# Optimization experiments

Hardware: AMD Instinct MI355X
Metric: run time of the kernel (lower is better)

## Reference

```python
import jax, jax.numpy as jnp
import numpy as np

N = 50000
E = 1_600_000
IN_C = 128
HID = 128
HEADS = 4
F_OUT = HID // HEADS  # 32
NEG_SLOPE = 0.2


def _glorot(key, shape):
    fan_in, fan_out = shape[0], shape[-1]
    lim = jnp.sqrt(6.0 / (fan_in + fan_out)).astype(jnp.float32)
    return jax.random.uniform(key, shape, jnp.float32, -lim, lim)


def setup_inputs() -> dict:
    key = jax.random.key(0)
    ks = jax.random.split(key, 12)
    x = jax.random.normal(ks[0], (N, IN_C), jnp.float32)
    edge_index = jax.random.randint(ks[1], (2, E), 0, N, jnp.int32)
    # layer 0 params
    W0 = _glorot(ks[2], (IN_C, HEADS * F_OUT))
    att_src0 = _glorot(ks[3], (HEADS, F_OUT))
    att_dst0 = _glorot(ks[4], (HEADS, F_OUT))
    b0 = jnp.zeros((HEADS * F_OUT,), jnp.float32)
    # layer 1 params
    W1 = _glorot(ks[5], (HID, HEADS * F_OUT))
    att_src1 = _glorot(ks[6], (HEADS, F_OUT))
    att_dst1 = _glorot(ks[7], (HEADS, F_OUT))
    b1 = jnp.zeros((HEADS * F_OUT,), jnp.float32)
    return {"x": x, "edge_index": edge_index,
            "W0": W0, "att_src0": att_src0, "att_dst0": att_dst0, "b0": b0,
            "W1": W1, "att_src1": att_src1, "att_dst1": att_dst1, "b1": b1}


def gat_conv(x, src, dst, W, att_src, att_dst, b):
    n = x.shape[0]
    h = (x @ W).reshape(n, HEADS, F_OUT)              # [N,H,F]
    a_s = jnp.einsum('nhf,hf->nh', h, att_src)        # [N,H]
    a_d = jnp.einsum('nhf,hf->nh', h, att_dst)        # [N,H]
    e = jax.nn.leaky_relu(a_s[src] + a_d[dst], NEG_SLOPE)   # [E,H]
    # segment softmax over destination-node neighborhoods
    e_max = jax.ops.segment_max(e, dst, num_segments=n)     # [N,H]
    e_exp = jnp.exp(e - e_max[dst])                          # [E,H]
    denom = jax.ops.segment_sum(e_exp, dst, num_segments=n)  # [N,H]
    denom = jnp.where(denom > 0, denom, 1.0)
    alpha = e_exp / denom[dst]                               # [E,H]
    msg = alpha[:, :, None] * h[src]                         # [E,H,F]
    out = jax.ops.segment_sum(msg, dst, num_segments=n)      # [N,H,F]
    return out.reshape(n, HEADS * F_OUT) + b


def reference(x, edge_index, W0, att_src0, att_dst0, b0, W1, att_src1, att_dst1, b1):
    src, dst = edge_index[0], edge_index[1]
    h = gat_conv(x, src, dst, W0, att_src0, att_dst0, b0)
    h = jax.nn.relu(h)  # dropout p=0.0 / eval mode -> identity
    out = gat_conv(h, src, dst, W1, att_src1, att_dst1, b1)
    return out
```

## Files before the change

kernel.cpp:

```cpp
#include <hip/hip_runtime.h>
#include <hip/hip_fp16.h>

#define N_NODES 50000
#define N_EDGES 1600000
#define NB 196
#define NBLK_H 256
#define CHUNK_H (N_EDGES / NBLK_H)
#define NBLK_S 512
#define CHUNK_S (N_EDGES / NBLK_S)
#define GEMM_BLOCKS 256

typedef _Float16 half8_t __attribute__((ext_vector_type(8)));
typedef _Float16 half2_t __attribute__((ext_vector_type(2)));
typedef float floatx4 __attribute__((ext_vector_type(4)));

#if defined(__has_builtin)
#  if __has_builtin(__builtin_amdgcn_fdot2)
#    define HAS_FDOT2 1
#  endif
#endif
#ifndef HAS_FDOT2
#  define HAS_FDOT2 0
#endif

__global__ __launch_bounds__(256) void edge_hist(const int* __restrict__ dst,
                                                 int* __restrict__ totals) {
    __shared__ int hist[NB];
    int t = threadIdx.x, b = blockIdx.x;
    if (t < NB) hist[t] = 0;
    __syncthreads();
    int s = b * CHUNK_H;
    for (int i = t; i < CHUNK_H; i += 256)
        atomicAdd(&hist[dst[s + i] >> 8], 1);
    __syncthreads();
    if (t < NB && hist[t]) atomicAdd(&totals[t], hist[t]);
}

__global__ __launch_bounds__(256) void gemm_mfma(const float* __restrict__ Xf,
                                                 const __half* __restrict__ Xh,
                                                 int in_half,
                                                 const float* __restrict__ W,
                                                 const float* __restrict__ att_s,
                                                 const float* __restrict__ att_d,
                                                 __half* __restrict__ H16,
                                                 float* __restrict__ as_out,
                                                 float* __restrict__ ad_out, int nrows,
                                                 const int* __restrict__ e_src,
                                                 const int* __restrict__ e_dst,
                                                 const int* __restrict__ btotal,
                                                 int* __restrict__ bcursor,
                                                 int* __restrict__ bucketed,
                                                 int with_scatter) {
    __shared__ __align__(16) char lds[49152];
    int t = threadIdx.x;
    if (with_scatter && blockIdx.x >= GEMM_BLOCKS) {
        int* recs   = reinterpret_cast<int*>(lds);
        int* srt    = reinterpret_cast<int*>(lds + 12800);
        int* bexcl  = reinterpret_cast<int*>(lds + 25600);
        int* hist   = reinterpret_cast<int*>(lds + 26624);
        int* lstart = reinterpret_cast<int*>(lds + 27648);
        int* curL   = reinterpret_cast<int*>(lds + 28672);
        int* gbase  = reinterpret_cast<int*>(lds + 29696);
        int b = blockIdx.x - GEMM_BLOCKS;
        int myTot = 0;
        if (t < NB) { myTot = btotal[t]; bexcl[t] = myTot; hist[t] = 0; }
        __syncthreads();
        for (int o = 1; o < NB; o <<= 1) {
            int v = (t < NB && t >= o) ? bexcl[t - o] : 0;
            __syncthreads();
            if (t < NB) bexcl[t] += v;
            __syncthreads();
        }
        if (t < NB) bexcl[t] -= myTot;
        int s0 = b * CHUNK_S;
        for (int i = t; i < CHUNK_S; i += 256) {
            unsigned sv = (unsigned)e_src[s0 + i], dv = (unsigned)e_dst[s0 + i];
            recs[i] = (int)((sv << 16) | dv);
            atomicAdd(&hist[dv >> 8], 1);
        }
        __syncthreads();
        int myCnt = (t < NB) ? hist[t] : 0;
        if (t < NB) lstart[t] = myCnt;
        __syncthreads();
        for (int o = 1; o < NB; o <<= 1) {
            int v = (t < NB && t >= o) ? lstart[t - o] : 0;
            __syncthreads();
            if (t < NB) lstart[t] += v;
            __syncthreads();
        }
        if (t < NB) {
            int ex = lstart[t] - myCnt;
            lstart[t] = ex;
            curL[t] = ex;
            gbase[t] = bexcl[t] + atomicAdd(&bcursor[t], myCnt);
        }
        __syncthreads();
        for (int i = t; i < CHUNK_S; i += 256) {
            int r = recs[i];
            int bk = (int)(((unsigned)r & 0xFFFFu) >> 8);
            int p = atomicAdd(&curL[bk], 1);
            srt[p] = r;
        }
        __syncthreads();
        for (int p = t; p < CHUNK_S; p += 256) {
            int r = srt[p];
            unsigned d = (unsigned)r & 0xFFFFu;
            int bk = (int)(d >> 8);
            int g = gbase[bk] + (p - lstart[bk]);
            bucketed[g] = (int)((((unsigned)r >> 16) << 8) | (d & 255u));
        }
        return;
    }
    char* Alds = lds;
    char* Wlds = lds + 16384;
    int lane = t & 63, wv_ = t >> 6;
    for (int p = 0; p < 16; ++p) {
        int flat = p * 256 + t;
        int k = flat >> 5;
        int n0 = (flat & 31) * 4;
        float4 wv = reinterpret_cast<const float4*>(W)[flat];
        const float* wf = reinterpret_cast<const float*>(&wv);
        #pragma unroll
        for (int i = 0; i < 4; ++i) {
            int n = n0 + i;
            int byte = (n * 256 + k * 2) ^ ((n & 7) << 4);
            *reinterpret_cast<__half*>(Wlds + byte) = __float2half(wf[i]);
        }
    }
    int col16 = lane & 15;
    float Asv[8], Adv[8];
    #pragma unroll
    for (int nt = 0; nt < 8; ++nt) {
        Asv[nt] = att_s[nt * 16 + col16];
        Adv[nt] = att_d[nt * 16 + col16];
    }
    int ksub = (lane >> 4) * 16;
    int rloc = wv_ * 16 + col16;
    int ntiles = (nrows + 63) / 64;
    for (int tile = blockIdx.x; tile < ntiles; tile += GEMM_BLOCKS) {
        int row0 = tile * 64;
        __syncthreads();
        for (int p = 0; p < 8; ++p) {
            int r = p * 8 + (t >> 5);
            int f4 = t & 31;
            int rr = row0 + r;
            uint2 hv = make_uint2(0, 0);
            if (rr < nrows) {
                if (in_half) {
                    hv = *reinterpret_cast<const uint2*>(Xh + (size_t)rr * 128 + f4 * 4);
                } else {
                    float4 xv = reinterpret_cast<const float4*>(Xf)[(size_t)rr * 32 + f4];
                    __half2* hp = reinterpret_cast<__half2*>(&hv);
                    hp[0] = __floats2half2_rn(xv.x, xv.y);
                    hp[1] = __floats2half2_rn(xv.z, xv.w);
                }
            }
            int byte = (r * 256 + f4 * 8) ^ ((r & 7) << 4);
            *reinterpret_cast<uint2*>(Alds + byte) = hv;
        }
        __syncthreads();
        half8_t afr[4];
        #pragma unroll
        for (int kb = 0; kb < 4; ++kb) {
            int byte = (rloc * 256 + kb * 64 + ksub) ^ ((rloc & 7) << 4);
            afr[kb] = *reinterpret_cast<half8_t*>(Alds + byte);
        }
        floatx4 acc[8];
        #pragma unroll
        for (int nt = 0; nt < 8; ++nt) {
            int n = nt * 16 + col16;
            floatx4 a = {0.f, 0.f, 0.f, 0.f};
            #pragma unroll
            for (int kb = 0; kb < 4; ++kb) {
                int byte = (n * 256 + kb * 64 + ksub) ^ ((n & 7) << 4);
                half8_t bfr = *reinterpret_cast<half8_t*>(Wlds + byte);
                a = __builtin_amdgcn_mfma_f32_16x16x32_f16(afr[kb], bfr, a, 0, 0, 0);
            }
            acc[nt] = a;
        }
        float ps[4][4], pd[4][4];
        #pragma unroll
        for (int reg = 0; reg < 4; ++reg)
            #pragma unroll
            for (int h = 0; h < 4; ++h) {
                ps[reg][h] = acc[2*h][reg] * Asv[2*h] + acc[2*h+1][reg] * Asv[2*h+1];
                pd[reg][h] = acc[2*h][reg] * Adv[2*h] + acc[2*h+1][reg] * Adv[2*h+1];
            }
        #pragma unroll
        for (int m = 1; m <= 8; m <<= 1)
            #pragma unroll
            for (int reg = 0; reg < 4; ++reg)
                #pragma unroll
                for (int h = 0; h < 4; ++h) {
                    ps[reg][h] += __shfl_xor(ps[reg][h], m);
                    pd[reg][h] += __shfl_xor(pd[reg][h], m);
                }
        int rbase = row0 + wv_ * 16 + (lane >> 4) * 4;
        #pragma unroll
        for (int reg = 0; reg < 4; ++reg) {
            int grow = rbase + reg;
            if (grow < nrows) {
                #pragma unroll
                for (int nt = 0; nt < 8; ++nt)
                    H16[(size_t)grow * 128 + nt * 16 + col16] = __float2half(acc[nt][reg]);
                if (col16 == 0) {
                    *reinterpret_cast<float4*>(as_out + (size_t)grow * 4) =
                        make_float4(ps[reg][0], ps[reg][1], ps[reg][2], ps[reg][3]);
                    *reinterpret_cast<float4*>(ad_out + (size_t)grow * 4) =
                        make_float4(pd[reg][0], pd[reg][1], pd[reg][2], pd[reg][3]);
                }
            }
        }
    }
}

__global__ __launch_bounds__(1024) void bucket_sort(const int* __restrict__ bucketed,
                                                    const int* __restrict__ btotal,
                                                    int* __restrict__ sorted_packed,
                                                    int* __restrict__ off) {
    __shared__ int bb[NB];
    __shared__ int cnt[256], scn[256], cur[256];
    int t = threadIdx.x, k = blockIdx.x;
    if (t < NB) bb[t] = btotal[t];
    if (t < 256) cnt[t] = 0;
    __syncthreads();
    for (int o = 1; o < NB; o <<= 1) {
        int v = (t < NB && t >= o) ? bb[t - o] : 0;
        __syncthreads();
        if (t < NB) bb[t] += v;
        __syncthreads();
    }
    int base = (k == 0) ? 0 : bb[k - 1];
    int end  = bb[k];
    int m = end - base;
    for (int i = t; i < m; i += 1024)
        atomicAdd(&cnt[bucketed[base + i] & 255], 1);
    __syncthreads();
    if (t < 256) scn[t] = cnt[t];
    __syncthreads();
    for (int o = 1; o < 256; o <<= 1) {
        int v = (t < 256 && t >= o) ? scn[t - o] : 0;
        __syncthreads();
        if (t < 256) scn[t] += v;
        __syncthreads();
    }
    if (t < 256) {
        int excl = scn[t] - cnt[t];
        cur[t] = base + excl;
        int node = k * 256 + t;
        if (node <= N_NODES) off[node] = base + excl;
    }
    __syncthreads();
    for (int i = t; i < m; i += 1024) {
        int rec = bucketed[base + i];
        int p = atomicAdd(&cur[rec & 255], 1);
        sorted_packed[p] = rec;
    }
}

__global__ __launch_bounds__(64, 8) void gat_aggregate_v4(const __half* __restrict__ H16,
                                                          const int* __restrict__ off,
                                                          const int* __restrict__ packed,
                                                          const float* __restrict__ asb,
                                                          const float* __restrict__ adb,
                                                          const float* __restrict__ bias,
                                                          float* __restrict__ OUTF,
                                                          __half* __restrict__ OUTH,
                                                          int n, int mode) {
    int wid = blockIdx.x;
    int lane = threadIdx.x;
    if (wid >= n) return;
    int s = off[wid], e = off[wid + 1];
    int q = lane >> 4;
    int sub = lane & 15;
    int head4 = (sub >> 2) * 4;
    int sub16 = sub * 16;
    float adv = adb[(size_t)wid * 4 + (sub >> 2)];
    const char* Hc = reinterpret_cast<const char*>(H16);
    const char* Ac = reinterpret_cast<const char*>(asb);
    float acc[8] = {0, 0, 0, 0, 0, 0, 0, 0};
    float den = 0.f;
    if (s < e) {
        int idx[4]; float sc[4];
        #pragma unroll
        for (int u = 0; u < 4; ++u) {
            int ii = s + q + u * 4;
            int jj = ii < e ? ii : s;
            idx[u] = packed[jj] & 0xFFFFFF00;
            sc[u] = *reinterpret_cast<const float*>(Ac + (idx[u] >> 4) + head4);
        }
        for (int i = s; i < e; i += 16) {
            uint4 h0 = *reinterpret_cast<const uint4*>(Hc + idx[0] + sub16);
            uint4 h1 = *reinterpret_cast<const uint4*>(Hc + idx[1] + sub16);
            uint4 h2 = *reinterpret_cast<const uint4*>(Hc + idx[2] + sub16);
            uint4 h3 = *reinterpret_cast<const uint4*>(Hc + idx[3] + sub16);
            float w[4];
            #pragma unroll
            for (int u = 0; u < 4; ++u) {
                float ev = sc[u] + adv; ev = fmaxf(ev, 0.2f * ev);
                w[u] = (i + q + u * 4 < e) ? __expf(ev) : 0.f;
            }
            #pragma unroll
            for (int u = 0; u < 4; ++u) {
                int ii = i + 16 + q + u * 4;
                int jj = ii < e ? ii : s;
                idx[u] = packed[jj] & 0xFFFFFF00;
                sc[u] = *reinterpret_cast<const float*>(Ac + (idx[u] >> 4) + head4);
            }
            den += (w[0] + w[1]) + (w[2] + w[3]);
#if HAS_FDOT2
            half2_t w01 = __builtin_bit_cast(half2_t, __builtin_amdgcn_cvt_pkrtz(w[0], w[1]));
            half2_t w23 = __builtin_bit_cast(half2_t, __builtin_amdgcn_cvt_pkrtz(w[2], w[3]));
            const uint* a0 = reinterpret_cast<const uint*>(&h0);
            const uint* a1 = reinterpret_cast<const uint*>(&h1);
            const uint* a2 = reinterpret_cast<const uint*>(&h2);
            const uint* a3 = reinterpret_cast<const uint*>(&h3);
            #pragma unroll
            for (int j = 0; j < 4; ++j) {
                uint p0 = __builtin_amdgcn_perm(a1[j], a0[j], 0x05040100u);
                uint p1 = __builtin_amdgcn_perm(a1[j], a0[j], 0x07060302u);
                uint r0 = __builtin_amdgcn_perm(a3[j], a2[j], 0x05040100u);
                uint r1 = __builtin_amdgcn_perm(a3[j], a2[j], 0x07060302u);
                acc[2*j]   = __builtin_amdgcn_fdot2(__builtin_bit_cast(half2_t, p0), w01,
                             __builtin_amdgcn_fdot2(__builtin_bit_cast(half2_t, r0), w23, acc[2*j],   false), false);
                acc[2*j+1] = __builtin_amdgcn_fdot2(__builtin_bit_cast(half2_t, p1), w01,
                             __builtin_amdgcn_fdot2(__builtin_bit_cast(half2_t, r1), w23, acc[2*j+1], false), false);
            }
#else
            const __half2* pa = reinterpret_cast<const __half2*>(&h0);
            const __half2* pb = reinterpret_cast<const __half2*>(&h1);
            const __half2* pc = reinterpret_cast<const __half2*>(&h2);
            const __half2* pd_ = reinterpret_cast<const __half2*>(&h3);
            #pragma unroll
            for (int j = 0; j < 4; ++j) {
                float2 fa = __half22float2(pa[j]);
                float2 fb = __half22float2(pb[j]);
                float2 fc = __half22float2(pc[j]);
                float2 fd = __half22float2(pd_[j]);
                acc[2*j]   += w[0] * fa.x + w[1] * fb.x + w[2] * fc.x + w[3] * fd.x;
                acc[2*j+1] += w[0] * fa.y + w[1] * fb.y + w[2] * fc.y + w[3] * fd.y;
            }
#endif
        }
    }
    #pragma unroll
    for (int j = 0; j < 8; ++j) acc[j] += __shfl_xor(acc[j], 16);
    den += __shfl_xor(den, 16);
    #pragma unroll
    for (int j = 0; j < 8; ++j) acc[j] += __shfl_xor(acc[j], 32);
    den += __shfl_xor(den, 32);
    if (q == 0) {
        float inv = den > 0.f ? 1.f / den : 0.f;
        float4 b0 = *reinterpret_cast<const float4*>(bias + sub * 8);
        float4 b1 = *reinterpret_cast<const float4*>(bias + sub * 8 + 4);
        float o[8];
        o[0] = acc[0]*inv + b0.x; o[1] = acc[1]*inv + b0.y;
        o[2] = acc[2]*inv + b0.z; o[3] = acc[3]*inv + b0.w;
        o[4] = acc[4]*inv + b1.x; o[5] = acc[5]*inv + b1.y;
        o[6] = acc[6]*inv + b1.z; o[7] = acc[7]*inv + b1.w;
        if (mode) {
            uint4 u;
            __half2* up = reinterpret_cast<__half2*>(&u);
            #pragma unroll
            for (int j = 0; j < 4; ++j)
                up[j] = __floats2half2_rn(fmaxf(o[2*j], 0.f), fmaxf(o[2*j+1], 0.f));
            *reinterpret_cast<uint4*>(OUTH + (size_t)wid * 128 + sub * 8) = u;
        } else {
            *reinterpret_cast<float4*>(OUTF + (size_t)wid * 128 + sub * 8) =
                make_float4(o[0], o[1], o[2], o[3]);
            *reinterpret_cast<float4*>(OUTF + (size_t)wid * 128 + sub * 8 + 4) =
                make_float4(o[4], o[5], o[6], o[7]);
        }
    }
}

extern "C" void kernel_launch(void* const* d_in, const int* in_sizes, int n_in,
                              void* d_out, int out_size, void* d_ws, size_t ws_size,
                              hipStream_t stream) {
    const float* x        = (const float*)d_in[0];
    const int*   edge     = (const int*)d_in[1];
    const float* W0       = (const float*)d_in[2];
    const float* att_src0 = (const float*)d_in[3];
    const float* att_dst0 = (const float*)d_in[4];
    const float* b0       = (const float*)d_in[5];
    const float* W1       = (const float*)d_in[6];
    const float* att_src1 = (const float*)d_in[7];
    const float* att_dst1 = (const float*)d_in[8];
    const float* b1       = (const float*)d_in[9];
    const int* src = edge;
    const int* dst = edge + N_EDGES;
    float* out = (float*)d_out;

    char* ws = (char*)d_ws;
    size_t o = 0;
    auto alloc = [&](size_t bytes) { char* p = ws + o; o += (bytes + 255) & ~(size_t)255; return p; };
    __half* H16   = (__half*)alloc((size_t)N_NODES * 128 * 2);
    float* asb    = (float*)alloc((size_t)N_NODES * 4 * 4);
    float* adb    = (float*)alloc((size_t)N_NODES * 4 * 4);
    int*   off    = (int*)alloc((size_t)(N_NODES + 1) * 4);
    int*   sorted = (int*)alloc((size_t)N_EDGES * 4);
    size_t mark = o;
    int*   btot2    = (int*)alloc((size_t)2 * NB * 4);
    int*   bucketed = (int*)alloc((size_t)N_EDGES * 4);
    (void)alloc((size_t)N_NODES * 128 * 2 > ((size_t)2*NB*4 + (size_t)N_EDGES*4)
                ? (size_t)N_NODES * 128 * 2 - ((size_t)2*NB*4 + 512 + (size_t)N_EDGES*4) : 0);
    __half* h1_16 = (__half*)(ws + mark);
    int* btotal  = btot2;
    int* bcursor = btot2 + NB;

    hipMemsetAsync(btot2, 0, (size_t)2 * NB * 4, stream);
    edge_hist<<<NBLK_H, 256, 0, stream>>>(dst, btotal);

    gemm_mfma<<<GEMM_BLOCKS + NBLK_S, 256, 0, stream>>>(x, (const __half*)nullptr, 0,
                                                        W0, att_src0, att_dst0,
                                                        H16, asb, adb, N_NODES,
                                                        src, dst, btotal, bcursor, bucketed, 1);
    bucket_sort<<<NB, 1024, 0, stream>>>(bucketed, btotal, sorted, off);

    gat_aggregate_v4<<<N_NODES, 64, 0, stream>>>(H16, off, sorted, asb, adb, b0,
                                                 (float*)nullptr, h1_16, N_NODES, 1);

    gemm_mfma<<<GEMM_BLOCKS, 256, 0, stream>>>((const float*)nullptr, h1_16, 1,
                                               W1, att_src1, att_dst1,
                                               H16, asb, adb, N_NODES,
                                               (const int*)nullptr, (const int*)nullptr,
                                               (const int*)nullptr, (int*)nullptr, (int*)nullptr, 0);
    gat_aggregate_v4<<<N_NODES, 64, 0, stream>>>(H16, off, sorted, asb, adb, b1,
                                                 out, (__half*)nullptr, N_NODES, 0);
}
```

Before: 207.8 us.

## Split node features into per-head planes and aggregate one head per wavefront

Features, the source and destination attention scores and the intermediate activations are now stored head-major, as four planes of N×32. The aggregation kernel assigns one wavefront to each (head, node) pair, and each head pass gathers only its 64-byte rows. The aim is to shrink the gathered working set per pass so it stays in cache, and to give the hardware more independent waves. In exchange each edge index is reloaded four times, there are more waves in total, and the fdot2 path and its 4-edge unrolled batching are dropped.

```diff
diff --git a/kernel.cpp b/kernel.cpp
--- a/kernel.cpp
+++ b/kernel.cpp
@@ -9,19 +9,10 @@
 #define NBLK_S 512
 #define CHUNK_S (N_EDGES / NBLK_S)
 #define GEMM_BLOCKS 256
+#define HPLANE (N_NODES * 32)
 
 typedef _Float16 half8_t __attribute__((ext_vector_type(8)));
-typedef _Float16 half2_t __attribute__((ext_vector_type(2)));
 typedef float floatx4 __attribute__((ext_vector_type(4)));
-
-#if defined(__has_builtin)
-#  if __has_builtin(__builtin_amdgcn_fdot2)
-#    define HAS_FDOT2 1
-#  endif
-#endif
-#ifndef HAS_FDOT2
-#  define HAS_FDOT2 0
-#endif
 
 __global__ __launch_bounds__(256) void edge_hist(const int* __restrict__ dst,
                                                  int* __restrict__ totals) {
@@ -42,9 +33,9 @@
                                                  const float* __restrict__ W,
                                                  const float* __restrict__ att_s,
                                                  const float* __restrict__ att_d,
-                                                 __half* __restrict__ H16,
-                                                 float* __restrict__ as_out,
-                                                 float* __restrict__ ad_out, int nrows,
+                                                 __half* __restrict__ Hh,
+                                                 float* __restrict__ ash,
+                                                 float* __restrict__ adh, int nrows,
                                                  const int* __restrict__ e_src,
                                                  const int* __restrict__ e_dst,
                                                  const int* __restrict__ btotal,
@@ -147,7 +138,9 @@
             uint2 hv = make_uint2(0, 0);
             if (rr < nrows) {
                 if (in_half) {
-                    hv = *reinterpret_cast<const uint2*>(Xh + (size_t)rr * 128 + f4 * 4);
+                    int col0 = f4 * 4;
+                    hv = *reinterpret_cast<const uint2*>(
+                        Xh + (size_t)(col0 >> 5) * HPLANE + (size_t)rr * 32 + (col0 & 31));
                 } else {
                     float4 xv = reinterpret_cast<const float4*>(Xf)[(size_t)rr * 32 + f4];
                     __half2* hp = reinterpret_cast<__half2*>(&hv);
@@ -201,13 +194,17 @@
             int grow = rbase + reg;
             if (grow < nrows) {
                 #pragma unroll
-                for (int nt = 0; nt < 8; ++nt)
-                    H16[(size_t)grow * 128 + nt * 16 + col16] = __float2half(acc[nt][reg]);
+                for (int nt = 0; nt < 8; ++nt) {
+                    int col = nt * 16 + col16;
+                    Hh[(size_t)(col >> 5) * HPLANE + (size_t)grow * 32 + (col & 31)] =
+                        __float2half(acc[nt][reg]);
+                }
                 if (col16 == 0) {
-                    *reinterpret_cast<float4*>(as_out + (size_t)grow * 4) =
-                        make_float4(ps[reg][0], ps[reg][1], ps[reg][2], ps[reg][3]);
-                    *reinterpret_cast<float4*>(ad_out + (size_t)grow * 4) =
-                        make_float4(pd[reg][0], pd[reg][1], pd[reg][2], pd[reg][3]);
+                    #pragma unroll
+                    for (int h = 0; h < 4; ++h) {
+                        ash[(size_t)h * N_NODES + grow] = ps[reg][h];
+                        adh[(size_t)h * N_NODES + grow] = pd[reg][h];
+                    }
                 }
             }
         }
@@ -258,101 +255,62 @@
     }
 }
 
-__global__ __launch_bounds__(64, 8) void gat_aggregate_v4(const __half* __restrict__ H16,
-                                                          const int* __restrict__ off,
-                                                          const int* __restrict__ packed,
-                                                          const float* __restrict__ asb,
-                                                          const float* __restrict__ adb,
-                                                          const float* __restrict__ bias,
-                                                          float* __restrict__ OUTF,
-                                                          __half* __restrict__ OUTH,
-                                                          int n, int mode) {
-    int wid = blockIdx.x;
-    int lane = threadIdx.x;
-    if (wid >= n) return;
+__global__ __launch_bounds__(256) void gat_aggregate_h(const __half* __restrict__ Hh,
+                                                       const int* __restrict__ off,
+                                                       const int* __restrict__ packed,
+                                                       const float* __restrict__ ash,
+                                                       const float* __restrict__ adh,
+                                                       const float* __restrict__ bias,
+                                                       float* __restrict__ OUTF,
+                                                       __half* __restrict__ OUTH,
+                                                       int mode) {
+    int w = (blockIdx.x * 256 + threadIdx.x) >> 6;
+    int lane = threadIdx.x & 63;
+    int p = w / N_NODES;
+    int wid = w - p * N_NODES;
     int s = off[wid], e = off[wid + 1];
-    int q = lane >> 4;
-    int sub = lane & 15;
-    int head4 = (sub >> 2) * 4;
-    int sub16 = sub * 16;
-    float adv = adb[(size_t)wid * 4 + (sub >> 2)];
-    const char* Hc = reinterpret_cast<const char*>(H16);
-    const char* Ac = reinterpret_cast<const char*>(asb);
+    int q = lane >> 2;
+    int sub = lane & 3;
+    const char* Hc = reinterpret_cast<const char*>(Hh) + (size_t)p * (N_NODES * 64);
+    const float* As = ash + (size_t)p * N_NODES;
+    float adv = adh[(size_t)p * N_NODES + wid];
     float acc[8] = {0, 0, 0, 0, 0, 0, 0, 0};
     float den = 0.f;
     if (s < e) {
-        int idx[4]; float sc[4];
-        #pragma unroll
-        for (int u = 0; u < 4; ++u) {
-            int ii = s + q + u * 4;
-            int jj = ii < e ? ii : s;
-            idx[u] = packed[jj] & 0xFFFFFF00;
-            sc[u] = *reinterpret_cast<const float*>(Ac + (idx[u] >> 4) + head4);
-        }
+        int ii = s + q;
+        int jj = ii < e ? ii : s;
+        int sidx = __builtin_nontemporal_load(packed + jj) >> 8;
+        float sc = As[sidx];
+        int rowb = sidx << 6;
         for (int i = s; i < e; i += 16) {
-            uint4 h0 = *reinterpret_cast<const uint4*>(Hc + idx[0] + sub16);
-            uint4 h1 = *reinterpret_cast<const uint4*>(Hc + idx[1] + sub16);
-            uint4 h2 = *reinterpret_cast<const uint4*>(Hc + idx[2] + sub16);
-            uint4 h3 = *reinterpret_cast<const uint4*>(Hc + idx[3] + sub16);
-            float w[4];
-            #pragma unroll
-            for (int u = 0; u < 4; ++u) {
-                float ev = sc[u] + adv; ev = fmaxf(ev, 0.2f * ev);
-                w[u] = (i + q + u * 4 < e) ? __expf(ev) : 0.f;
-            }
-            #pragma unroll
-            for (int u = 0; u < 4; ++u) {
-                int ii = i + 16 + q + u * 4;
-                int jj = ii < e ? ii : s;
-                idx[u] = packed[jj] & 0xFFFFFF00;
-                sc[u] = *reinterpret_cast<const float*>(Ac + (idx[u] >> 4) + head4);
-            }
-            den += (w[0] + w[1]) + (w[2] + w[3]);
-#if HAS_FDOT2
-            half2_t w01 = __builtin_bit_cast(half2_t, __builtin_amdgcn_cvt_pkrtz(w[0], w[1]));
-            half2_t w23 = __builtin_bit_cast(half2_t, __builtin_amdgcn_cvt_pkrtz(w[2], w[3]));
-            const uint* a0 = reinterpret_cast<const uint*>(&h0);
-            const uint* a1 = reinterpret_cast<const uint*>(&h1);
-            const uint* a2 = reinterpret_cast<const uint*>(&h2);
-            const uint* a3 = reinterpret_cast<const uint*>(&h3);
+            uint4 hv = *reinterpret_cast<const uint4*>(Hc + rowb + sub * 16);
+            float ev = sc + adv; ev = fmaxf(ev, 0.2f * ev);
+            float w0 = (i + q < e) ? __expf(ev) : 0.f;
+            int ii2 = i + 16 + q;
+            int jj2 = ii2 < e ? ii2 : s;
+            sidx = __builtin_nontemporal_load(packed + jj2) >> 8;
+            sc = As[sidx];
+            rowb = sidx << 6;
+            den += w0;
+            const __half2* ph = reinterpret_cast<const __half2*>(&hv);
             #pragma unroll
             for (int j = 0; j < 4; ++j) {
-                uint p0 = __builtin_amdgcn_perm(a1[j], a0[j], 0x05040100u);
-                uint p1 = __builtin_amdgcn_perm(a1[j], a0[j], 0x07060302u);
-                uint r0 = __builtin_amdgcn_perm(a3[j], a2[j], 0x05040100u);
-                uint r1 = __builtin_amdgcn_perm(a3[j], a2[j], 0x07060302u);
-                acc[2*j]   = __builtin_amdgcn_fdot2(__builtin_bit_cast(half2_t, p0), w01,
-                             __builtin_amdgcn_fdot2(__builtin_bit_cast(half2_t, r0), w23, acc[2*j],   false), false);
-                acc[2*j+1] = __builtin_amdgcn_fdot2(__builtin_bit_cast(half2_t, p1), w01,
-                             __builtin_amdgcn_fdot2(__builtin_bit_cast(half2_t, r1), w23, acc[2*j+1], false), false);
-            }
-#else
-            const __half2* pa = reinterpret_cast<const __half2*>(&h0);
-            const __half2* pb = reinterpret_cast<const __half2*>(&h1);
-            const __half2* pc = reinterpret_cast<const __half2*>(&h2);
-            const __half2* pd_ = reinterpret_cast<const __half2*>(&h3);
-            #pragma unroll
-            for (int j = 0; j < 4; ++j) {
-                float2 fa = __half22float2(pa[j]);
-                float2 fb = __half22float2(pb[j]);
-                float2 fc = __half22float2(pc[j]);
-                float2 fd = __half22float2(pd_[j]);
-                acc[2*j]   += w[0] * fa.x + w[1] * fb.x + w[2] * fc.x + w[3] * fd.x;
-                acc[2*j+1] += w[0] * fa.y + w[1] * fb.y + w[2] * fc.y + w[3] * fd.y;
-            }
-#endif
+                float2 f = __half22float2(ph[j]);
+                acc[2*j]   += w0 * f.x;
+                acc[2*j+1] += w0 * f.y;
+            }
         }
     }
     #pragma unroll
-    for (int j = 0; j < 8; ++j) acc[j] += __shfl_xor(acc[j], 16);
-    den += __shfl_xor(den, 16);
-    #pragma unroll
-    for (int j = 0; j < 8; ++j) acc[j] += __shfl_xor(acc[j], 32);
-    den += __shfl_xor(den, 32);
+    for (int m = 4; m <= 32; m <<= 1) {
+        #pragma unroll
+        for (int j = 0; j < 8; ++j) acc[j] += __shfl_xor(acc[j], m);
+        den += __shfl_xor(den, m);
+    }
     if (q == 0) {
         float inv = den > 0.f ? 1.f / den : 0.f;
-        float4 b0 = *reinterpret_cast<const float4*>(bias + sub * 8);
-        float4 b1 = *reinterpret_cast<const float4*>(bias + sub * 8 + 4);
+        float4 b0 = *reinterpret_cast<const float4*>(bias + p * 32 + sub * 8);
+        float4 b1 = *reinterpret_cast<const float4*>(bias + p * 32 + sub * 8 + 4);
         float o[8];
         o[0] = acc[0]*inv + b0.x; o[1] = acc[1]*inv + b0.y;
         o[2] = acc[2]*inv + b0.z; o[3] = acc[3]*inv + b0.w;
@@ -364,11 +322,11 @@
             #pragma unroll
             for (int j = 0; j < 4; ++j)
                 up[j] = __floats2half2_rn(fmaxf(o[2*j], 0.f), fmaxf(o[2*j+1], 0.f));
-            *reinterpret_cast<uint4*>(OUTH + (size_t)wid * 128 + sub * 8) = u;
+            *reinterpret_cast<uint4*>(OUTH + (size_t)p * HPLANE + (size_t)wid * 32 + sub * 8) = u;
         } else {
-            *reinterpret_cast<float4*>(OUTF + (size_t)wid * 128 + sub * 8) =
+            *reinterpret_cast<float4*>(OUTF + (size_t)wid * 128 + p * 32 + sub * 8) =
                 make_float4(o[0], o[1], o[2], o[3]);
-            *reinterpret_cast<float4*>(OUTF + (size_t)wid * 128 + sub * 8 + 4) =
+            *reinterpret_cast<float4*>(OUTF + (size_t)wid * 128 + p * 32 + sub * 8 + 4) =
                 make_float4(o[4], o[5], o[6], o[7]);
         }
     }
@@ -394,17 +352,16 @@
     char* ws = (char*)d_ws;
     size_t o = 0;
     auto alloc = [&](size_t bytes) { char* p = ws + o; o += (bytes + 255) & ~(size_t)255; return p; };
-    __half* H16   = (__half*)alloc((size_t)N_NODES * 128 * 2);
-    float* asb    = (float*)alloc((size_t)N_NODES * 4 * 4);
-    float* adb    = (float*)alloc((size_t)N_NODES * 4 * 4);
+    __half* Hh    = (__half*)alloc((size_t)N_NODES * 128 * 2);
+    float* ash    = (float*)alloc((size_t)4 * N_NODES * 4);
+    float* adh    = (float*)alloc((size_t)4 * N_NODES * 4);
     int*   off    = (int*)alloc((size_t)(N_NODES + 1) * 4);
     int*   sorted = (int*)alloc((size_t)N_EDGES * 4);
     size_t mark = o;
     int*   btot2    = (int*)alloc((size_t)2 * NB * 4);
     int*   bucketed = (int*)alloc((size_t)N_EDGES * 4);
-    (void)alloc((size_t)N_NODES * 128 * 2 > ((size_t)2*NB*4 + (size_t)N_EDGES*4)
-                ? (size_t)N_NODES * 128 * 2 - ((size_t)2*NB*4 + 512 + (size_t)N_EDGES*4) : 0);
-    __half* h1_16 = (__half*)(ws + mark);
+    o = mark + (size_t)N_NODES * 128 * 2;
+    __half* h1h = (__half*)(ws + mark);
     int* btotal  = btot2;
     int* bcursor = btot2 + NB;
 
@@ -413,18 +370,18 @@
 
     gemm_mfma<<<GEMM_BLOCKS + NBLK_S, 256, 0, stream>>>(x, (const __half*)nullptr, 0,
                                                         W0, att_src0, att_dst0,
-                                                        H16, asb, adb, N_NODES,
+                                                        Hh, ash, adh, N_NODES,
                                                         src, dst, btotal, bcursor, bucketed, 1);
     bucket_sort<<<NB, 1024, 0, stream>>>(bucketed, btotal, sorted, off);
 
-    gat_aggregate_v4<<<N_NODES, 64, 0, stream>>>(H16, off, sorted, asb, adb, b0,
-                                                 (float*)nullptr, h1_16, N_NODES, 1);
-
-    gemm_mfma<<<GEMM_BLOCKS, 256, 0, stream>>>((const float*)nullptr, h1_16, 1,
+    gat_aggregate_h<<<N_NODES, 256, 0, stream>>>(Hh, off, sorted, ash, adh, b0,
+                                                 (float*)nullptr, h1h, 1);
+
+    gemm_mfma<<<GEMM_BLOCKS, 256, 0, stream>>>((const float*)nullptr, h1h, 1,
                                                W1, att_src1, att_dst1,
-                                               H16, asb, adb, N_NODES,
+                                               Hh, ash, adh, N_NODES,
                                                (const int*)nullptr, (const int*)nullptr,
                                                (const int*)nullptr, (int*)nullptr, (int*)nullptr, 0);
-    gat_aggregate_v4<<<N_NODES, 64, 0, stream>>>(H16, off, sorted, asb, adb, b1,
-                                                 out, (__half*)nullptr, N_NODES, 0);
-}
+    gat_aggregate_h<<<N_NODES, 256, 0, stream>>>(Hh, off, sorted, ash, adh, b1,
+                                                 out, (__half*)nullptr, 0);
+}
```

Result: slower. 328.3 us (+58.0%).
